# Kernel optimization log

Hardware: AMD Instinct MI355X
Metric: run time of the kernel (lower is better)

## Reference

```python
import jax, jax.numpy as jnp
import numpy as np

BS, NS, D, H = 4, 1024, 2048, 16
DH = D // H
SCALE = DH ** -0.5
MASK_BIAS = -1e9


def setup_inputs() -> dict:
    key = jax.random.key(0)
    k1, k2, k3, k4, k5 = jax.random.split(key, 5)
    x = jax.random.normal(k1, (BS, NS, D), dtype=jnp.float32)
    attention_ids = jax.random.randint(k2, (BS, NS), 0, 2, dtype=jnp.int32)
    # torch.nn.Linear weights: [out_features, in_features]
    w_in = jax.random.normal(k3, (3 * D, D), dtype=jnp.float32) * (D ** -0.5)
    w_out = jax.random.normal(k4, (D, D), dtype=jnp.float32) * (D ** -0.5)
    b_out = jax.random.normal(k5, (D,), dtype=jnp.float32) * 0.02
    return {"x": x, "attention_ids": attention_ids, "w_in": w_in,
            "w_out": w_out, "b_out": b_out}


def reference(x, attention_ids, w_in, w_out, b_out):
    bs, ns, _ = x.shape
    qkv = jnp.einsum('bsd,ed->bse', x, w_in)            # [bs, ns, 3*D]
    qkv = qkv.reshape(bs, ns, 3, H, DH).transpose(2, 0, 3, 1, 4)
    q, k, v = qkv[0], qkv[1], qkv[2]                     # [bs, H, ns, DH]
    attn = jnp.einsum('bhqd,bhkd->bhqk', q, k)           # [bs, H, ns, ns]
    # NOTE: mask bias added BEFORE the scale multiply, as in the source.
    bias = (attention_ids.astype(attn.dtype) * MASK_BIAS)[:, None, None, :]
    attn = jax.nn.softmax((attn + bias) * SCALE, axis=-1)
    out = jnp.einsum('bhqk,bhkd->bhqd', attn, v)         # [bs, H, ns, DH]
    out = out.transpose(0, 2, 1, 3).reshape(bs, ns, D)
    return jnp.einsum('bsd,ed->bse', out, w_out) + b_out
```

## Files before the change

kernel.cpp:

```cpp
#include <hip/hip_runtime.h>
#include <hip/hip_bf16.h>
#include <stdint.h>

typedef __bf16 bf16;
typedef __bf16 bf16x8 __attribute__((ext_vector_type(8)));
typedef __bf16 bf16x4 __attribute__((ext_vector_type(4)));
typedef float floatx4 __attribute__((ext_vector_type(4)));

#define NSEQ   1024
#define DM     2048
#define NH     16
#define DHD    128
#define E3     6144
#define SCALE_F 0.08838834764831845f
#define MBIAS_S (-1.0e9f * SCALE_F)
#define NEG_HUGE (-3.0e38f)

static __device__ __forceinline__ floatx4 mfma16(bf16x8 a, bf16x8 b, floatx4 c) {
  return __builtin_amdgcn_mfma_f32_16x16x32_bf16(a, b, c, 0, 0, 0);
}

static __device__ __forceinline__ void load_lds16(const bf16* g, bf16* l) {
  __builtin_amdgcn_global_load_lds(
      (__attribute__((address_space(1))) const void*)g,
      (__attribute__((address_space(3))) void*)l, 16, 0, 0);
}

__global__ __launch_bounds__(256) void cast_bf16_kernel(const float* __restrict__ in,
                                                        bf16* __restrict__ out) {
  int i = blockIdx.x * 256 + threadIdx.x;
  float4 v = ((const float4*)in)[i];
  bf16x4 o;
  o[0] = (bf16)v.x; o[1] = (bf16)v.y; o[2] = (bf16)v.z; o[3] = (bf16)v.w;
  ((bf16x4*)out)[i] = o;
}

template <typename OutT>
__global__ __launch_bounds__(256) void gemm_bt_kernel(
    const bf16* __restrict__ A, const bf16* __restrict__ B,
    OutT* __restrict__ C, const float* __restrict__ bias,
    int N, int K) {
  __shared__ bf16 As[128 * 32];
  __shared__ bf16 Bs[128 * 32];
  const int ntn = N >> 7;
  const int tm = blockIdx.x / ntn;
  const int tn = blockIdx.x - tm * ntn;
  const int tid = threadIdx.x;
  const int w = tid >> 6;
  const int lane = tid & 63;
  const int lq = lane & 15;
  const int lg = lane >> 4;
  const int wr = w >> 1;
  const int wc = w & 1;

  const bf16* Ag = A + (size_t)(tm * 128) * K;
  const bf16* Bg = B + (size_t)(tn * 128) * K;
  const int c0 = tid, c1 = tid + 256;
  const int r0 = c0 >> 2, o0 = (c0 & 3) * 8;
  const int r1 = c1 >> 2, o1 = (c1 & 3) * 8;
  bf16* lA0 = As + w * 512;
  bf16* lA1 = As + w * 512 + 2048;
  bf16* lB0 = Bs + w * 512;
  bf16* lB1 = Bs + w * 512 + 2048;

  floatx4 acc[4][4] = {};

  for (int k0 = 0; k0 < K; k0 += 32) {
    load_lds16(Ag + (size_t)r0 * K + k0 + o0, lA0);
    load_lds16(Ag + (size_t)r1 * K + k0 + o1, lA1);
    load_lds16(Bg + (size_t)r0 * K + k0 + o0, lB0);
    load_lds16(Bg + (size_t)r1 * K + k0 + o1, lB1);
    __syncthreads();
    bf16x8 af[4], bfr[4];
#pragma unroll
    for (int m = 0; m < 4; m++)
      af[m] = *(const bf16x8*)(As + (wr * 64 + m * 16 + lq) * 32 + lg * 8);
#pragma unroll
    for (int n = 0; n < 4; n++)
      bfr[n] = *(const bf16x8*)(Bs + (wc * 64 + n * 16 + lq) * 32 + lg * 8);
#pragma unroll
    for (int m = 0; m < 4; m++)
#pragma unroll
      for (int n = 0; n < 4; n++)
        acc[m][n] = mfma16(af[m], bfr[n], acc[m][n]);
    __syncthreads();
  }

#pragma unroll
  for (int n = 0; n < 4; n++) {
    const int ccol = tn * 128 + wc * 64 + n * 16 + lq;
    const float bv = bias ? bias[ccol] : 0.f;
#pragma unroll
    for (int m = 0; m < 4; m++) {
      const size_t rbase = (size_t)(tm * 128 + wr * 64 + m * 16 + lg * 4);
#pragma unroll
      for (int r = 0; r < 4; r++)
        C[(rbase + r) * N + ccol] = (OutT)(acc[m][n][r] + bv);
    }
  }
}

__global__ __launch_bounds__(256) void vtrans_kernel(const bf16* __restrict__ qkv,
                                                     bf16* __restrict__ vt) {
  const int bid = blockIdx.x;
  const int sblk = bid & 7;
  const int h = (bid >> 3) & 15;
  const int b = bid >> 7;
  const int t = threadIdx.x;
  const int dhb = (t & 7) | (((t >> 6) & 1) << 3);
  const int sb  = ((t >> 3) & 7) | (((t >> 7) & 1) << 3);
  const int s0 = sblk * 128 + sb * 8;
  const int dh0 = dhb * 8;
  const bf16* src = qkv + (size_t)(b * NSEQ + s0) * E3 + 2 * DM + h * DHD + dh0;
  bf16x8 r[8];
#pragma unroll
  for (int i = 0; i < 8; i++) r[i] = *(const bf16x8*)(src + (size_t)i * E3);
  bf16* dst = vt + ((size_t)(b * NH + h) * DHD + dh0) * NSEQ + s0;
#pragma unroll
  for (int j = 0; j < 8; j++) {
    bf16x8 o;
#pragma unroll
    for (int i = 0; i < 8; i++) o[i] = r[i][j];
    *(bf16x8*)(dst + (size_t)j * NSEQ) = o;
  }
}

__global__ __launch_bounds__(256) void attn_kernel(
    const bf16* __restrict__ qkv, const bf16* __restrict__ vt,
    const int* __restrict__ ids, bf16* __restrict__ ao) {
  __shared__ bf16 Ksh[2][64 * 128];
  __shared__ bf16 Vsh[2][128 * 64];
  __shared__ bf16 plds[4][16][72];
  const int bid = blockIdx.x;
  const int qt = bid & 15;
  const int h = (bid >> 4) & 15;
  const int b = bid >> 8;
  const int tid = threadIdx.x;
  const int w = tid >> 6;
  const int lane = tid & 63;
  const int lq = lane & 15;
  const int lg = lane >> 4;
  const int q0 = qt * 64 + w * 16;
  const int swz = (lq & 7) << 4;

  const int krow0 = w * 16 + (lane >> 4);
  const int kc = lane & 15;
  const int vrow0 = w * 32 + (lane >> 3);
  const int vc = lane & 7;
  const int vr7 = (lane >> 3) & 7;

  const bf16* kg = qkv + DM + h * DHD;
  const bf16* vg = vt + (size_t)(b * NH + h) * DHD * NSEQ;

  auto stage = [&](int buf, int k0) {
#pragma unroll
    for (int i = 0; i < 4; i++) {
      const int kr = krow0 + i * 4;
      load_lds16(kg + (size_t)(b * NSEQ + k0 + kr) * E3 + ((kc ^ (kr & 7)) * 8),
                 &Ksh[buf][(w * 16 + i * 4) * 128]);
    }
#pragma unroll
    for (int i = 0; i < 4; i++) {
      const int vr = vrow0 + i * 8;
      load_lds16(vg + (size_t)vr * NSEQ + k0 + ((vc ^ vr7) * 8),
                 &Vsh[buf][(w * 32 + i * 8) * 64]);
    }
  };

  bf16x8 qf[4];
  const bf16* qb = qkv + (size_t)(b * NSEQ + q0 + lq) * E3 + h * DHD + lg * 8;
#pragma unroll
  for (int kk = 0; kk < 4; kk++) qf[kk] = *(const bf16x8*)(qb + kk * 32);

  floatx4 acc[8] = {};
  float M[4], L[4];
#pragma unroll
  for (int r = 0; r < 4; r++) { M[r] = NEG_HUGE; L[r] = 0.f; }

  bf16 (*pw)[72] = plds[w];
  const int* idb = ids + b * NSEQ;

  stage(0, 0);
  __syncthreads();
  int cur = 0;

  for (int t = 0; t < 16; t++) {
    const int k0 = t * 64;
    if (t < 15) stage(cur ^ 1, k0 + 64);

    const bf16* Kc = Ksh[cur];
    floatx4 s[4] = {};
#pragma unroll
    for (int n = 0; n < 4; n++) {
      const int krow = n * 16 + lq;
#pragma unroll
      for (int kk = 0; kk < 4; kk++) {
        bf16x8 kf = *(const bf16x8*)(Kc + krow * 128 +
                                     (((kk * 64 + lg * 16) ^ swz) >> 1));
        s[n] = mfma16(qf[kk], kf, s[n]);
      }
    }
    float sa[4][4], pm[4];
#pragma unroll
    for (int r = 0; r < 4; r++) pm[r] = NEG_HUGE;
#pragma unroll
    for (int n = 0; n < 4; n++) {
      const float bv = idb[k0 + n * 16 + lq] ? MBIAS_S : 0.f;
#pragma unroll
      for (int r = 0; r < 4; r++) {
        sa[n][r] = s[n][r] * SCALE_F + bv;
        pm[r] = fmaxf(pm[r], sa[n][r]);
      }
    }
#pragma unroll
    for (int m = 1; m <= 8; m <<= 1)
#pragma unroll
      for (int r = 0; r < 4; r++) pm[r] = fmaxf(pm[r], __shfl_xor(pm[r], m, 64));
    float corr[4];
#pragma unroll
    for (int r = 0; r < 4; r++) {
      const float mn = fmaxf(M[r], pm[r]);
      corr[r] = __expf(M[r] - mn);
      M[r] = mn;
    }
    float rs[4] = {0.f, 0.f, 0.f, 0.f};
#pragma unroll
    for (int n = 0; n < 4; n++)
#pragma unroll
      for (int r = 0; r < 4; r++) {
        const float p = __expf(sa[n][r] - M[r]);
        sa[n][r] = p;
        rs[r] += p;
      }
#pragma unroll
    for (int m = 1; m <= 8; m <<= 1)
#pragma unroll
      for (int r = 0; r < 4; r++) rs[r] += __shfl_xor(rs[r], m, 64);
#pragma unroll
    for (int r = 0; r < 4; r++) L[r] = L[r] * corr[r] + rs[r];
#pragma unroll
    for (int n8 = 0; n8 < 8; n8++)
#pragma unroll
      for (int r = 0; r < 4; r++) acc[n8][r] *= corr[r];
#pragma unroll
    for (int n = 0; n < 4; n++)
#pragma unroll
      for (int r = 0; r < 4; r++) pw[lg * 4 + r][n * 16 + lq] = (bf16)sa[n][r];
    bf16x8 pf0 = *(const bf16x8*)(&pw[lq][lg * 8]);
    bf16x8 pf1 = *(const bf16x8*)(&pw[lq][32 + lg * 8]);
    const bf16* Vc = Vsh[cur];
#pragma unroll
    for (int n8 = 0; n8 < 8; n8++) {
      const int vrow = n8 * 16 + lq;
      bf16x8 v0 = *(const bf16x8*)(Vc + vrow * 64 + (((lg * 16) ^ swz) >> 1));
      bf16x8 v1 = *(const bf16x8*)(Vc + vrow * 64 + (((64 + lg * 16) ^ swz) >> 1));
      acc[n8] = mfma16(pf0, v0, acc[n8]);
      acc[n8] = mfma16(pf1, v1, acc[n8]);
    }
    __syncthreads();
    cur ^= 1;
  }

  float inv[4];
#pragma unroll
  for (int r = 0; r < 4; r++) inv[r] = 1.f / L[r];
  bf16* aob = ao + (size_t)(b * NSEQ + q0 + lg * 4) * DM + h * DHD + lq;
#pragma unroll
  for (int n8 = 0; n8 < 8; n8++)
#pragma unroll
    for (int r = 0; r < 4; r++)
      aob[(size_t)r * DM + n8 * 16] = (bf16)(acc[n8][r] * inv[r]);
}

extern "C" void kernel_launch(void* const* d_in, const int* in_sizes, int n_in,
                              void* d_out, int out_size, void* d_ws, size_t ws_size,
                              hipStream_t stream) {
  const float* x     = (const float*)d_in[0];
  const int*   ids   = (const int*)d_in[1];
  const float* w_in  = (const float*)d_in[2];
  const float* w_out = (const float*)d_in[3];
  const float* b_out = (const float*)d_in[4];
  float* out = (float*)d_out;

  bf16* ws  = (bf16*)d_ws;
  bf16* xb  = ws;
  bf16* wib = xb  + (size_t)4096 * 2048;
  bf16* wob = wib + (size_t)6144 * 2048;
  bf16* qkv = wob + (size_t)2048 * 2048;
  bf16* vtb = qkv + (size_t)4096 * 6144;
  bf16* aob = vtb + (size_t)4 * 16 * 128 * 1024;

  cast_bf16_kernel<<<8192, 256, 0, stream>>>(x, xb);
  cast_bf16_kernel<<<12288, 256, 0, stream>>>(w_in, wib);
  cast_bf16_kernel<<<4096, 256, 0, stream>>>(w_out, wob);
  gemm_bt_kernel<bf16><<<32 * 48, 256, 0, stream>>>(xb, wib, qkv, nullptr, 6144, 2048);
  vtrans_kernel<<<512, 256, 0, stream>>>(qkv, vtb);
  attn_kernel<<<1024, 256, 0, stream>>>(qkv, vtb, ids, aob);
  gemm_bt_kernel<float><<<32 * 16, 256, 0, stream>>>(aob, wob, out, b_out, 2048, 2048);
}
```

Measured before the change: 323.3 us.

## Add 256x256-tile pipelined GEMM with 512 threads for QKV projection

Adds a new GEMM kernel with 256x256 output tiles and 8 waves. It double-buffers K-slices in LDS through direct global-to-LDS loads, uses an XOR-swizzled layout, and interleaves staging with MFMA phases behind explicit barriers, waitcnts and setprio. The QKV projection now uses this kernel instead of the 128x128 one. The intent is more data reuse per tile and loads hidden behind compute. The cost is only 384 blocks for 256 CUs, which gives poor wave balance, plus heavy register use for 32 accumulators.

New measurement: 325.8 us. No clear change (+0.8%).

```diff
diff --git a/kernel.cpp b/kernel.cpp
--- a/kernel.cpp
+++ b/kernel.cpp
@@ -26,6 +26,8 @@
       (__attribute__((address_space(3))) void*)l, 16, 0, 0);
 }
 
+#define SCHED0 __builtin_amdgcn_sched_barrier(0)
+
 __global__ __launch_bounds__(256) void cast_bf16_kernel(const float* __restrict__ in,
                                                         bf16* __restrict__ out) {
   int i = blockIdx.x * 256 + threadIdx.x;
@@ -33,6 +35,140 @@
   bf16x4 o;
   o[0] = (bf16)v.x; o[1] = (bf16)v.y; o[2] = (bf16)v.z; o[3] = (bf16)v.w;
   ((bf16x4*)out)[i] = o;
+}
+
+template <typename OutT>
+__global__ __launch_bounds__(512) void gemm256_bt_kernel(
+    const bf16* __restrict__ A, const bf16* __restrict__ B,
+    OutT* __restrict__ C, const float* __restrict__ bias,
+    int N, int K) {
+  __shared__ __align__(16) bf16 Al[2][2][256 * 32];
+  __shared__ __align__(16) bf16 Bl[2][2][256 * 32];
+  const int NT = K >> 6;
+  const int ntn = N >> 8;
+  const int tm = blockIdx.x / ntn;
+  const int tn = blockIdx.x - tm * ntn;
+  const int tid = threadIdx.x;
+  const int w = tid >> 6, lane = tid & 63;
+  const int lq = lane & 15, lg = lane >> 4;
+  const int wr = w >> 2, wc = w & 3;
+  const int sub = lane >> 2;
+  const int cpl = (lane & 3) ^ ((lane >> 3) & 3);
+  const int scp8 = (lg ^ ((lq >> 1) & 3)) << 3;
+
+  const bf16* Ag = A + (size_t)(tm * 256) * K;
+  const bf16* Bg = B + (size_t)(tn * 256) * K;
+
+  auto STAGE = [&](const bf16* G, bf16* Ldst, int kcol) {
+#pragma unroll
+    for (int j = 0; j < 2; j++) {
+      const int r0 = w * 32 + j * 16;
+      load_lds16(G + (size_t)(r0 + sub) * K + kcol + cpl * 8, Ldst + r0 * 32);
+    }
+  };
+  auto RD = [&](const bf16* slot, int rbase) -> bf16x8 {
+    return *(const bf16x8*)(slot + (rbase + lq) * 32 + scp8);
+  };
+
+  floatx4 acc[8][4] = {};
+
+  STAGE(Ag, Al[0][0], 0);
+  STAGE(Bg, Bl[0][0], 0);
+  STAGE(Ag, Al[0][1], 32);
+  STAGE(Bg, Bl[0][1], 32);
+  STAGE(Ag, Al[1][0], 64);
+  STAGE(Bg, Bl[1][0], 64);
+  asm volatile("s_waitcnt vmcnt(4)" ::: "memory");
+  SCHED0;
+  __builtin_amdgcn_s_barrier();
+  SCHED0;
+
+  int buf = 0;
+  for (int kt = 0; kt < NT; ++kt) {
+    const int nb = buf ^ 1;
+    const int k1 = ((kt + 1 < NT) ? kt + 1 : NT - 1) << 6;
+    const int k2 = ((kt + 2 < NT) ? kt + 2 : NT - 1) << 6;
+    bf16x8 af[4], bfr[4];
+
+#pragma unroll
+    for (int ni = 0; ni < 4; ni++) bfr[ni] = RD(Bl[buf][0], wc * 64 + ni * 16);
+#pragma unroll
+    for (int mi = 0; mi < 4; mi++) af[mi] = RD(Al[buf][0], wr * 128 + mi * 16);
+    STAGE(Ag, Al[nb][1], k1 + 32);
+    SCHED0; __builtin_amdgcn_s_barrier();
+    asm volatile("s_waitcnt lgkmcnt(0)" ::: "memory"); SCHED0;
+    __builtin_amdgcn_s_setprio(1);
+#pragma unroll
+    for (int mi = 0; mi < 4; mi++)
+#pragma unroll
+      for (int ni = 0; ni < 4; ni++)
+        acc[mi][ni] = mfma16(af[mi], bfr[ni], acc[mi][ni]);
+    __builtin_amdgcn_s_setprio(0);
+    SCHED0; __builtin_amdgcn_s_barrier(); SCHED0;
+
+#pragma unroll
+    for (int mi = 0; mi < 4; mi++)
+      af[mi] = RD(Al[buf][0], wr * 128 + (4 + mi) * 16);
+    STAGE(Bg, Bl[nb][1], k1 + 32);
+    SCHED0; __builtin_amdgcn_s_barrier();
+    asm volatile("s_waitcnt lgkmcnt(0)" ::: "memory"); SCHED0;
+    __builtin_amdgcn_s_setprio(1);
+#pragma unroll
+    for (int mi = 0; mi < 4; mi++)
+#pragma unroll
+      for (int ni = 0; ni < 4; ni++)
+        acc[4 + mi][ni] = mfma16(af[mi], bfr[ni], acc[4 + mi][ni]);
+    __builtin_amdgcn_s_setprio(0);
+    SCHED0; __builtin_amdgcn_s_barrier(); SCHED0;
+
+#pragma unroll
+    for (int ni = 0; ni < 4; ni++) bfr[ni] = RD(Bl[buf][1], wc * 64 + ni * 16);
+#pragma unroll
+    for (int mi = 0; mi < 4; mi++) af[mi] = RD(Al[buf][1], wr * 128 + mi * 16);
+    STAGE(Ag, Al[buf][0], k2);
+    SCHED0; __builtin_amdgcn_s_barrier();
+    asm volatile("s_waitcnt lgkmcnt(0)" ::: "memory"); SCHED0;
+    __builtin_amdgcn_s_setprio(1);
+#pragma unroll
+    for (int mi = 0; mi < 4; mi++)
+#pragma unroll
+      for (int ni = 0; ni < 4; ni++)
+        acc[mi][ni] = mfma16(af[mi], bfr[ni], acc[mi][ni]);
+    __builtin_amdgcn_s_setprio(0);
+    SCHED0; __builtin_amdgcn_s_barrier(); SCHED0;
+
+#pragma unroll
+    for (int mi = 0; mi < 4; mi++)
+      af[mi] = RD(Al[buf][1], wr * 128 + (4 + mi) * 16);
+    STAGE(Bg, Bl[buf][0], k2);
+    SCHED0; __builtin_amdgcn_s_barrier();
+    asm volatile("s_waitcnt lgkmcnt(0)" ::: "memory"); SCHED0;
+    __builtin_amdgcn_s_setprio(1);
+#pragma unroll
+    for (int mi = 0; mi < 4; mi++)
+#pragma unroll
+      for (int ni = 0; ni < 4; ni++)
+        acc[4 + mi][ni] = mfma16(af[mi], bfr[ni], acc[4 + mi][ni]);
+    __builtin_amdgcn_s_setprio(0);
+    asm volatile("s_waitcnt vmcnt(4)" ::: "memory");
+    SCHED0; __builtin_amdgcn_s_barrier(); SCHED0;
+
+    buf = nb;
+  }
+  asm volatile("s_waitcnt vmcnt(0)" ::: "memory");
+
+#pragma unroll
+  for (int ni = 0; ni < 4; ni++) {
+    const int col = tn * 256 + wc * 64 + ni * 16 + lq;
+    const float bv = bias ? bias[col] : 0.f;
+#pragma unroll
+    for (int m = 0; m < 8; m++) {
+      const size_t rb = (size_t)(tm * 256 + wr * 128 + m * 16 + lg * 4);
+#pragma unroll
+      for (int r = 0; r < 4; r++)
+        C[(rb + r) * N + col] = (OutT)(acc[m][ni][r] + bv);
+    }
+  }
 }
 
 template <typename OutT>
@@ -293,7 +429,7 @@
   cast_bf16_kernel<<<8192, 256, 0, stream>>>(x, xb);
   cast_bf16_kernel<<<12288, 256, 0, stream>>>(w_in, wib);
   cast_bf16_kernel<<<4096, 256, 0, stream>>>(w_out, wob);
-  gemm_bt_kernel<bf16><<<32 * 48, 256, 0, stream>>>(xb, wib, qkv, nullptr, 6144, 2048);
+  gemm256_bt_kernel<bf16><<<16 * 24, 512, 0, stream>>>(xb, wib, qkv, nullptr, 6144, 2048);
   vtrans_kernel<<<512, 256, 0, stream>>>(qkv, vtb);
   attn_kernel<<<1024, 256, 0, stream>>>(qkv, vtb, ids, aob);
   gemm_bt_kernel<float><<<32 * 16, 256, 0, stream>>>(aob, wob, out, b_out, 2048, 2048);
```
